# Kernel tuning notes

Measured on AMD Instinct MI355X. Metric: run time of the kernel, lower is better.

The kernel has to match this reference:

```python
import jax, jax.numpy as jnp
import numpy as np

N = 50000
E = 800000
IN = 256
H = 4
C = 64
HC = H * C
LAT = 64
EPS = 1e-5
NEG_SLOPE = 0.2


def setup_inputs() -> dict:
    key = jax.random.key(0)
    ks = jax.random.split(key, 20)
    g = lambda k, shape, fan: jax.random.normal(k, shape, jnp.float32) * (1.0 / np.sqrt(fan))
    return {
        "x": jax.random.normal(ks[0], (N, IN), jnp.float32),
        "edge_index": jax.random.randint(ks[1], (2, E), 0, N, jnp.int32),
        "Wl1": g(ks[2], (IN, HC), IN), "Wr1": g(ks[3], (IN, HC), IN),
        "att1": g(ks[4], (H, C), C), "b1": jnp.zeros((HC,), jnp.float32),
        "ln1_g": jnp.ones((HC,), jnp.float32), "ln1_b": jnp.zeros((HC,), jnp.float32),
        "Wl2": g(ks[5], (HC, HC), HC), "Wr2": g(ks[6], (HC, HC), HC),
        "att2": g(ks[7], (H, C), C), "b2": jnp.zeros((HC,), jnp.float32),
        "ln2_g": jnp.ones((HC,), jnp.float32), "ln2_b": jnp.zeros((HC,), jnp.float32),
        "Wmu": g(ks[8], (HC, LAT), HC), "bmu": jnp.zeros((LAT,), jnp.float32),
        "Wlv": g(ks[9], (HC, LAT), HC), "blv": jnp.zeros((LAT,), jnp.float32),
    }


def _gatv2_layer(x, src, dst, Wl, Wr, att, bias):
    # GATv2: e_ij = att . leaky_relu(Wl x_j + Wr x_i); segment softmax over dst; aggregate Wl x_j
    xl = (x @ Wl).reshape(-1, H, C)  # source transform [N,H,C]
    xr = (x @ Wr).reshape(-1, H, C)  # target transform [N,H,C]
    e = jax.nn.leaky_relu(xl[src] + xr[dst], NEG_SLOPE)   # [E',H,C]
    score = jnp.einsum('ehc,hc->eh', e, att)              # [E',H]
    m = jax.ops.segment_max(score, dst, num_segments=N)   # [N,H]
    ex = jnp.exp(score - m[dst])
    denom = jax.ops.segment_sum(ex, dst, num_segments=N)  # [N,H]
    alpha = ex / denom[dst]                               # self-loops guarantee denom > 0
    out = jax.ops.segment_sum(alpha[:, :, None] * xl[src], dst, num_segments=N)  # [N,H,C]
    return out.reshape(-1, HC) + bias


def _layernorm(x, g, b):
    mu = jnp.mean(x, axis=-1, keepdims=True)
    var = jnp.mean((x - mu) ** 2, axis=-1, keepdims=True)
    return (x - mu) * jax.lax.rsqrt(var + EPS) * g + b


def reference(x, edge_index, Wl1, Wr1, att1, b1, ln1_g, ln1_b,
              Wl2, Wr2, att2, b2, ln2_g, ln2_b, Wmu, bmu, Wlv, blv):
    loops = jnp.arange(N, dtype=edge_index.dtype)
    src = jnp.concatenate([edge_index[0], loops])  # add_self_loops=True
    dst = jnp.concatenate([edge_index[1], loops])
    h = _gatv2_layer(x, src, dst, Wl1, Wr1, att1, b1)
    h = jax.nn.elu(_layernorm(h, ln1_g, ln1_b))  # dropout is identity in eval mode
    h = _gatv2_layer(h, src, dst, Wl2, Wr2, att2, b2)
    h = jax.nn.elu(_layernorm(h, ln2_g, ln2_b))
    mu = h @ Wmu + bmu
    logvar = h @ Wlv + blv
    return mu, logvar
```

## Files before the change

kernel.cpp:

```cpp
#include <hip/hip_runtime.h>
#include <hip/hip_bf16.h>

#define NN 50000
#define NE 800000
#define HCn 256
#define LATn 64

typedef short bf16x4 __attribute__((ext_vector_type(4)));
typedef short bf16x8 __attribute__((ext_vector_type(8)));
typedef float f32x4 __attribute__((ext_vector_type(4)));

__device__ __forceinline__ short f2b(float f) {
    __hip_bfloat16 h = __float2bfloat16(f);
    return __builtin_bit_cast(short, h);
}
__device__ __forceinline__ float b2f(short s) {
    return __bfloat162float(__builtin_bit_cast(__hip_bfloat16, s));
}

#define SWZF(v, pat) __builtin_bit_cast(float, __builtin_amdgcn_ds_swizzle(__builtin_bit_cast(int, v), pat))

#define C04L2E 0.5770780163555854f
#define C06L2E 0.8656170245333781f
#define DEFER_THR 8.0f

__global__ void hist_kernel(const int* __restrict__ dst, int* __restrict__ counts) {
    int e = blockIdx.x * 256 + threadIdx.x;
    if (e < NE) atomicAdd(&counts[dst[e]], 1);
}

__global__ __launch_bounds__(1024) void scan1_kernel(int* __restrict__ counts,
                                                     int* __restrict__ blocksum) {
    const int g = blockIdx.x * 1024 + threadIdx.x;
    const int lane = threadIdx.x & 63;
    const int wv = threadIdx.x >> 6;
    int v = (g < NN) ? counts[g] : 0;
    int s = v;
#pragma unroll
    for (int d = 1; d < 64; d <<= 1) {
        int t = __shfl_up(s, d, 64);
        if (lane >= d) s += t;
    }
    __shared__ int wsum[16];
    if (lane == 63) wsum[wv] = s;
    __syncthreads();
    if (threadIdx.x == 0) {
        int run = 0;
#pragma unroll
        for (int q = 0; q < 16; ++q) { int t = wsum[q]; wsum[q] = run; run += t; }
        blocksum[blockIdx.x] = run;
    }
    __syncthreads();
    int excl = s - v + wsum[wv];
    if (g < NN) counts[g] = excl;
}

__global__ void scan2_kernel(int* __restrict__ blocksum, int* __restrict__ offsets, int nblk) {
    const int lane = threadIdx.x;
    int v = (lane < nblk) ? blocksum[lane] : 0;
    int s = v;
#pragma unroll
    for (int d = 1; d < 64; d <<= 1) {
        int t = __shfl_up(s, d, 64);
        if (lane >= d) s += t;
    }
    if (lane < nblk) blocksum[lane] = s - v;
    if (lane == 0) offsets[NN] = NE;
}

__global__ __launch_bounds__(1024) void scan3_kernel(const int* __restrict__ counts,
                                                     const int* __restrict__ blocksum,
                                                     int* __restrict__ offsets,
                                                     int* __restrict__ cursor) {
    const int g = blockIdx.x * 1024 + threadIdx.x;
    if (g < NN) {
        int v = counts[g] + blocksum[blockIdx.x];
        offsets[g] = v;
        cursor[g]  = v;
    }
}

__global__ void scatter_kernel(const int* __restrict__ src, const int* __restrict__ dst,
                               int* __restrict__ cursor, int* __restrict__ csr_src) {
    int e = blockIdx.x * 256 + threadIdx.x;
    if (e < NE) {
        int p = atomicAdd(&cursor[dst[e]], 1);
        csr_src[p] = src[e];
    }
}

__global__ void pack_w_kernel(const float* __restrict__ Wl1, const float* __restrict__ Wr1,
                              const float* __restrict__ Wl2, const float* __restrict__ Wr2,
                              const float* __restrict__ Wmu, const float* __restrict__ Wlv,
                              const float* __restrict__ bmu, const float* __restrict__ blv,
                              short* __restrict__ Wb1t, short* __restrict__ Wb2t,
                              short* __restrict__ Wb3t, float* __restrict__ bias3) {
    int i = blockIdx.x * 256 + threadIdx.x;
    const int S1 = 512 * 256, S2 = 2 * S1, S3 = S2 + 128 * 256;
    if (i < S1) {
        int c = i >> 8, k = i & 255;
        float v = (c < 256) ? Wl1[k * 256 + c] : Wr1[k * 256 + (c - 256)];
        Wb1t[i] = f2b(v);
    } else if (i < S2) {
        int j = i - S1; int c = j >> 8, k = j & 255;
        float v = (c < 256) ? Wl2[k * 256 + c] : Wr2[k * 256 + (c - 256)];
        Wb2t[j] = f2b(v);
    } else if (i < S3) {
        int j = i - S2; int c = j >> 8, k = j & 255;
        float v = (c < 64) ? Wmu[k * 64 + c] : Wlv[k * 64 + (c - 64)];
        Wb3t[j] = f2b(v);
    } else if (i < S3 + 128) {
        int c = i - S3;
        bias3[c] = (c < 64) ? bmu[c] : blv[c - 64];
    }
}

template<int A_F32, int OUT_MODE>
__global__ __launch_bounds__(256) void gemm_k(
    const void* __restrict__ Ap, const short* __restrict__ Wbt,
    void* __restrict__ outp, const float* __restrict__ bias, int Nc)
{
    __shared__ short Bs[128 * 256];
    const int t = threadIdx.x;
    const int w = t >> 6, lane = t & 63;
    const int row0 = blockIdx.x * 128, col0 = blockIdx.y * 128;

    {
        const int sn = t >> 1;
        const int half = t & 1;
        const short* wp = Wbt + (long)(col0 + sn) * 256 + half * 128;
        short* bp = &Bs[sn * 256];
        const int sx = sn & 7;
#pragma unroll
        for (int r = 0; r < 16; ++r) {
            bf16x8 v = *reinterpret_cast<const bf16x8*>(wp + r * 8);
            int c = half * 16 + r;
            *reinterpret_cast<bf16x8*>(bp + ((c ^ sx) * 8)) = v;
        }
    }
    __syncthreads();

    f32x4 acc[2][8];
#pragma unroll
    for (int a = 0; a < 2; ++a)
#pragma unroll
        for (int b = 0; b < 8; ++b) acc[a][b] = (f32x4){0.f, 0.f, 0.f, 0.f};

    const int arow = lane & 15, kq = lane >> 4;
    const int xorc = arow & 7;
    int r0 = row0 + w * 32 + arow;      if (r0 > NN - 1) r0 = NN - 1;
    int r1 = row0 + w * 32 + 16 + arow; if (r1 > NN - 1) r1 = NN - 1;

#pragma unroll
    for (int k0 = 0; k0 < 256; k0 += 32) {
        bf16x8 a0, a1;
        if (A_F32) {
            const float* A = (const float*)Ap;
            const f32x4* q0 = reinterpret_cast<const f32x4*>(A + (long)r0 * 256 + kq * 8 + k0);
            const f32x4* q1 = reinterpret_cast<const f32x4*>(A + (long)r1 * 256 + kq * 8 + k0);
            f32x4 u0 = q0[0], u1 = q0[1], v0 = q1[0], v1 = q1[1];
#pragma unroll
            for (int j = 0; j < 4; ++j) {
                a0[j] = f2b(u0[j]); a0[4 + j] = f2b(u1[j]);
                a1[j] = f2b(v0[j]); a1[4 + j] = f2b(v1[j]);
            }
        } else {
            const short* A = (const short*)Ap;
            a0 = *reinterpret_cast<const bf16x8*>(A + (long)r0 * 256 + kq * 8 + k0);
            a1 = *reinterpret_cast<const bf16x8*>(A + (long)r1 * 256 + kq * 8 + k0);
        }
        const int chunk = ((k0 >> 3) + kq) ^ xorc;
        const short* bsp = &Bs[arow * 256 + chunk * 8];
#pragma unroll
        for (int nt = 0; nt < 8; ++nt) {
            bf16x8 b = *reinterpret_cast<const bf16x8*>(bsp + nt * 4096);
            acc[0][nt] = __builtin_amdgcn_mfma_f32_16x16x32_bf16(a0, b, acc[0][nt], 0, 0, 0);
            acc[1][nt] = __builtin_amdgcn_mfma_f32_16x16x32_bf16(a1, b, acc[1][nt], 0, 0, 0);
        }
    }

#pragma unroll
    for (int rb = 0; rb < 2; ++rb)
#pragma unroll
        for (int nt = 0; nt < 8; ++nt) {
            int gcol = col0 + nt * 16 + arow;
#pragma unroll
            for (int r = 0; r < 4; ++r) {
                int grow = row0 + w * 32 + rb * 16 + kq * 4 + r;
                if (grow < NN) {
                    float v = acc[rb][nt][r];
                    if (OUT_MODE == 0) {
                        ((short*)outp)[(long)grow * Nc + gcol] = f2b(v);
                    } else {
                        v += bias[gcol];
                        float* o = (float*)outp;
                        if (gcol < 64) o[(long)grow * 64 + gcol] = v;
                        else           o[(long)NN * 64 + (long)grow * 64 + (gcol - 64)] = v;
                    }
                }
            }
        }
}

__global__ __launch_bounds__(256) void att_pre_kernel(
    const short* __restrict__ xlr, const float* __restrict__ att, float* __restrict__ a)
{
    const int i = blockIdx.x * 4 + (threadIdx.x >> 6);
    const int lane = threadIdx.x & 63;
    const int c4 = (lane >> 4) * 64 + (lane & 15) * 4;
    f32x4 attv = *reinterpret_cast<const f32x4*>(att + c4);
    bf16x4 v = *reinterpret_cast<const bf16x4*>(xlr + (long)i * 512 + c4);
    float s = 0.f;
#pragma unroll
    for (int k = 0; k < 4; ++k) s = fmaf(b2f(v[k]), attv[k], s);
    s += SWZF(s, 0x041F);
    s += SWZF(s, 0x081F);
    s += SWZF(s, 0x101F);
    s += SWZF(s, 0x201F);
    if ((lane & 15) == 0) a[i * 4 + (lane >> 4)] = s * C06L2E;
}

__device__ __forceinline__ void edge_abs_score(const short* __restrict__ xlr, int j, int c4,
                                               const float* xr, const f32x4& attv04,
                                               float* xf, float& s) {
    bf16x4 v = *reinterpret_cast<const bf16x4*>(xlr + (long)j * 512 + c4);
    s = 0.f;
#pragma unroll
    for (int k = 0; k < 4; ++k) {
        xf[k] = b2f(v[k]);
        float vv = xf[k] + xr[k];
        s = fmaf(attv04[k], fabsf(vv), s);
    }
    s += SWZF(s, 0x041F);
    s += SWZF(s, 0x081F);
    s += SWZF(s, 0x101F);
    s += SWZF(s, 0x201F);
}

__global__ __launch_bounds__(256) void gat_node_kernel(
    const short* __restrict__ xlr, const float* __restrict__ aarr,
    const int* __restrict__ offsets, const int* __restrict__ csr_src,
    const float* __restrict__ att, const float* __restrict__ bias,
    const float* __restrict__ ln_g, const float* __restrict__ ln_b,
    short* __restrict__ hout)
{
    const int i = blockIdx.x * 4 + (threadIdx.x >> 6);
    const int lane = threadIdx.x & 63;
    const int h  = lane >> 4;
    const int c4 = h * 64 + (lane & 15) * 4;

    f32x4 attv04 = *reinterpret_cast<const f32x4*>(att + c4);
#pragma unroll
    for (int k = 0; k < 4; ++k) attv04[k] *= C04L2E;

    float xr[4];
    {
        bf16x4 v = *reinterpret_cast<const bf16x4*>(xlr + (long)i * 512 + 256 + c4);
#pragma unroll
        for (int k = 0; k < 4; ++k) xr[k] = b2f(v[k]);
    }

    const int p0 = offsets[i], p1 = offsets[i + 1];

    int pp = p0 + (lane & 3);
    int jl = csr_src[pp < NE ? pp : NE - 1];

    float m, l;
    float acc[4];
    {
        float aj = aarr[i * 4 + h];
        float xf[4], s;
        edge_abs_score(xlr, i, c4, xr, attv04, xf, s);
        m = s + aj; l = 1.f;
#pragma unroll
        for (int k = 0; k < 4; ++k) acc[k] = xf[k];
    }

    int p = p0;
    for (; p + 4 <= p1; p += 4) {
        int j0 = __builtin_amdgcn_readlane(jl, 0);
        int j1 = __builtin_amdgcn_readlane(jl, 1);
        int j2 = __builtin_amdgcn_readlane(jl, 2);
        int j3 = __builtin_amdgcn_readlane(jl, 3);
        int pn = p + 4 + (lane & 3);
        jl = csr_src[pn < p1 ? pn : (p1 > 0 ? p1 - 1 : 0)];
        float a0 = aarr[j0 * 4 + h], a1 = aarr[j1 * 4 + h];
        float a2 = aarr[j2 * 4 + h], a3 = aarr[j3 * 4 + h];
        float x0[4], x1[4], x2[4], x3[4], s0, s1, s2, s3;
        edge_abs_score(xlr, j0, c4, xr, attv04, x0, s0);
        edge_abs_score(xlr, j1, c4, xr, attv04, x1, s1);
        edge_abs_score(xlr, j2, c4, xr, attv04, x2, s2);
        edge_abs_score(xlr, j3, c4, xr, attv04, x3, s3);
        s0 += a0; s1 += a1; s2 += a2; s3 += a3;
        float sm = fmaxf(fmaxf(s0, s1), fmaxf(s2, s3));
        if (__all(sm <= m + DEFER_THR)) {
            float e0 = __builtin_amdgcn_exp2f(s0 - m);
            float e1 = __builtin_amdgcn_exp2f(s1 - m);
            float e2 = __builtin_amdgcn_exp2f(s2 - m);
            float e3 = __builtin_amdgcn_exp2f(s3 - m);
            l += (e0 + e1) + (e2 + e3);
#pragma unroll
            for (int k = 0; k < 4; ++k)
                acc[k] = fmaf(e0, x0[k], fmaf(e1, x1[k], fmaf(e2, x2[k], fmaf(e3, x3[k], acc[k]))));
        } else {
            float mn = fmaxf(m, sm);
            float corr = __builtin_amdgcn_exp2f(m - mn);
            float e0 = __builtin_amdgcn_exp2f(s0 - mn);
            float e1 = __builtin_amdgcn_exp2f(s1 - mn);
            float e2 = __builtin_amdgcn_exp2f(s2 - mn);
            float e3 = __builtin_amdgcn_exp2f(s3 - mn);
            l = fmaf(l, corr, (e0 + e1) + (e2 + e3));
#pragma unroll
            for (int k = 0; k < 4; ++k)
                acc[k] = fmaf(acc[k], corr,
                         fmaf(e0, x0[k], fmaf(e1, x1[k], fmaf(e2, x2[k], e3 * x3[k]))));
            m = mn;
        }
    }
    int rem = p1 - p;
    for (int tq = 0; tq < rem; ++tq) {
        int j = __builtin_amdgcn_readlane(jl, tq);
        float aj = aarr[j * 4 + h];
        float xa[4], sa;
        edge_abs_score(xlr, j, c4, xr, attv04, xa, sa);
        sa += aj;
        if (__all(sa <= m + DEFER_THR)) {
            float ex = __builtin_amdgcn_exp2f(sa - m);
            l += ex;
#pragma unroll
            for (int k = 0; k < 4; ++k) acc[k] = fmaf(ex, xa[k], acc[k]);
        } else {
            float mn = fmaxf(m, sa);
            float corr = __builtin_amdgcn_exp2f(m - mn);
            float ex = __builtin_amdgcn_exp2f(sa - mn);
            l = fmaf(l, corr, ex);
#pragma unroll
            for (int k = 0; k < 4; ++k) acc[k] = fmaf(acc[k], corr, ex * xa[k]);
            m = mn;
        }
    }

    float inv = 1.f / l;
    f32x4 bv = *reinterpret_cast<const f32x4*>(bias + c4);
    float out[4], s1 = 0.f, s2 = 0.f;
#pragma unroll
    for (int k = 0; k < 4; ++k) {
        out[k] = acc[k] * inv + bv[k];
        s1 += out[k];
        s2 += out[k] * out[k];
    }
    s1 += SWZF(s1, 0x041F); s2 += SWZF(s2, 0x041F);
    s1 += SWZF(s1, 0x081F); s2 += SWZF(s2, 0x081F);
    s1 += SWZF(s1, 0x101F); s2 += SWZF(s2, 0x101F);
    s1 += SWZF(s1, 0x201F); s2 += SWZF(s2, 0x201F);
    s1 += SWZF(s1, 0x401F); s2 += SWZF(s2, 0x401F);
    s1 += __shfl_xor(s1, 32, 64);
    s2 += __shfl_xor(s2, 32, 64);
    float mu  = s1 * (1.f / 256.f);
    float var = s2 * (1.f / 256.f) - mu * mu;
    float rs  = rsqrtf(var + 1e-5f);
    f32x4 gv  = *reinterpret_cast<const f32x4*>(ln_g + c4);
    f32x4 bbv = *reinterpret_cast<const f32x4*>(ln_b + c4);
    bf16x4 o;
#pragma unroll
    for (int k = 0; k < 4; ++k) {
        float y = (out[k] - mu) * rs * gv[k] + bbv[k];
        y = y > 0.f ? y : expm1f(y);
        o[k] = f2b(y);
    }
    *reinterpret_cast<bf16x4*>(hout + (long)i * 256 + c4) = o;
}

extern "C" void kernel_launch(void* const* d_in, const int* in_sizes, int n_in,
                              void* d_out, int out_size, void* d_ws, size_t ws_size,
                              hipStream_t stream) {
    const float* x    = (const float*)d_in[0];
    const int*   ei   = (const int*)d_in[1];
    const float* Wl1  = (const float*)d_in[2];
    const float* Wr1  = (const float*)d_in[3];
    const float* att1 = (const float*)d_in[4];
    const float* b1   = (const float*)d_in[5];
    const float* ln1g = (const float*)d_in[6];
    const float* ln1b = (const float*)d_in[7];
    const float* Wl2  = (const float*)d_in[8];
    const float* Wr2  = (const float*)d_in[9];
    const float* att2 = (const float*)d_in[10];
    const float* b2   = (const float*)d_in[11];
    const float* ln2g = (const float*)d_in[12];
    const float* ln2b = (const float*)d_in[13];
    const float* Wmu  = (const float*)d_in[14];
    const float* bmu  = (const float*)d_in[15];
    const float* Wlv  = (const float*)d_in[16];
    const float* blv  = (const float*)d_in[17];

    short* bufXL = (short*)d_ws;
    short* bufH  = bufXL + (long)NN * 512;
    short* Wb1t  = bufH + (long)NN * 256;
    short* Wb2t  = Wb1t + 512 * 256;
    short* Wb3t  = Wb2t + 512 * 256;
    float* bias3 = (float*)(Wb3t + 128 * 256);
    int* counts  = (int*)(bias3 + 128);
    int* offsets = counts + NN;
    int* cursor  = offsets + NN + 1;
    int* csr_src = cursor + NN;
    int* blocksum = csr_src + NE;
    float* a_arr = (float*)(blocksum + 64);

    const int* src = ei;
    const int* dst = ei + NE;

    const int NBLK = (NN + 1023) / 1024;

    hipMemsetAsync(counts, 0, NN * sizeof(int), stream);
    hist_kernel<<<(NE + 255) / 256, 256, 0, stream>>>(dst, counts);
    scan1_kernel<<<NBLK, 1024, 0, stream>>>(counts, blocksum);
    scan2_kernel<<<1, 64, 0, stream>>>(blocksum, offsets, NBLK);
    scan3_kernel<<<NBLK, 1024, 0, stream>>>(counts, blocksum, offsets, cursor);
    scatter_kernel<<<(NE + 255) / 256, 256, 0, stream>>>(src, dst, cursor, csr_src);

    pack_w_kernel<<<1153, 256, 0, stream>>>(Wl1, Wr1, Wl2, Wr2, Wmu, Wlv, bmu, blv,
                                            Wb1t, Wb2t, Wb3t, bias3);

    const int GM = (NN + 127) / 128;
    dim3 g1(GM, 4);
    dim3 g3(GM, 1);

    gemm_k<1, 0><<<g1, 256, 0, stream>>>(x, Wb1t, bufXL, nullptr, 512);
    att_pre_kernel<<<NN / 4, 256, 0, stream>>>(bufXL, att1, a_arr);
    gat_node_kernel<<<NN / 4, 256, 0, stream>>>(bufXL, a_arr, offsets, csr_src,
                                                att1, b1, ln1g, ln1b, bufH);
    gemm_k<0, 0><<<g1, 256, 0, stream>>>(bufH, Wb2t, bufXL, nullptr, 512);
    att_pre_kernel<<<NN / 4, 256, 0, stream>>>(bufXL, att2, a_arr);
    gat_node_kernel<<<NN / 4, 256, 0, stream>>>(bufXL, a_arr, offsets, csr_src,
                                                att2, b2, ln2g, ln2b, bufH);
    gemm_k<0, 1><<<g3, 256, 0, stream>>>(bufH, Wb3t, d_out, bias3, 128);
}
```

Measured before the change: 374.0 us.

## Restructure GEMM to hold A rows in registers and fuse attention precompute

The GEMM now keeps each block's 64-row A tile in registers and loops over all output column tiles, staging a 64-column weight slice in shared memory per iteration. This replaces the earlier 2D grid that re-read A once per column tile. The separate att_pre kernel is removed: its per-node attention dot product is computed from the fp32 accumulators inside the GEMM epilogue, saving one launch and a re-read of the bf16 output per layer. In exchange, the column loop is serialised with a barrier per tile, there are fewer independent blocks, and the attention term now comes from unrounded fp32 values rather than the stored bf16 ones.

```diff
diff --git a/kernel.cpp b/kernel.cpp
--- a/kernel.cpp
+++ b/kernel.cpp
@@ -115,80 +115,98 @@
     }
 }
 
-template<int A_F32, int OUT_MODE>
+template<int A_F32, int OUT_MODE, int NCT, int ATT>
 __global__ __launch_bounds__(256) void gemm_k(
     const void* __restrict__ Ap, const short* __restrict__ Wbt,
-    void* __restrict__ outp, const float* __restrict__ bias, int Nc)
+    void* __restrict__ outp, const float* __restrict__ bias,
+    const float* __restrict__ att, float* __restrict__ a_arr, int Nc)
 {
-    __shared__ short Bs[128 * 256];
+    __shared__ short Bs[64 * 256];
     const int t = threadIdx.x;
     const int w = t >> 6, lane = t & 63;
-    const int row0 = blockIdx.x * 128, col0 = blockIdx.y * 128;
-
-    {
-        const int sn = t >> 1;
-        const int half = t & 1;
-        const short* wp = Wbt + (long)(col0 + sn) * 256 + half * 128;
-        short* bp = &Bs[sn * 256];
-        const int sx = sn & 7;
-#pragma unroll
-        for (int r = 0; r < 16; ++r) {
-            bf16x8 v = *reinterpret_cast<const bf16x8*>(wp + r * 8);
-            int c = half * 16 + r;
-            *reinterpret_cast<bf16x8*>(bp + ((c ^ sx) * 8)) = v;
-        }
-    }
-    __syncthreads();
-
-    f32x4 acc[2][8];
-#pragma unroll
-    for (int a = 0; a < 2; ++a)
-#pragma unroll
-        for (int b = 0; b < 8; ++b) acc[a][b] = (f32x4){0.f, 0.f, 0.f, 0.f};
-
+    const int row0 = blockIdx.x * 64;
     const int arow = lane & 15, kq = lane >> 4;
     const int xorc = arow & 7;
-    int r0 = row0 + w * 32 + arow;      if (r0 > NN - 1) r0 = NN - 1;
-    int r1 = row0 + w * 32 + 16 + arow; if (r1 > NN - 1) r1 = NN - 1;
-
-#pragma unroll
-    for (int k0 = 0; k0 < 256; k0 += 32) {
-        bf16x8 a0, a1;
+
+    bf16x8 af[8];
+    {
+        int r0 = row0 + w * 16 + arow; if (r0 > NN - 1) r0 = NN - 1;
         if (A_F32) {
             const float* A = (const float*)Ap;
-            const f32x4* q0 = reinterpret_cast<const f32x4*>(A + (long)r0 * 256 + kq * 8 + k0);
-            const f32x4* q1 = reinterpret_cast<const f32x4*>(A + (long)r1 * 256 + kq * 8 + k0);
-            f32x4 u0 = q0[0], u1 = q0[1], v0 = q1[0], v1 = q1[1];
-#pragma unroll
-            for (int j = 0; j < 4; ++j) {
-                a0[j] = f2b(u0[j]); a0[4 + j] = f2b(u1[j]);
-                a1[j] = f2b(v0[j]); a1[4 + j] = f2b(v1[j]);
+            const float* base = A + (long)r0 * 256 + kq * 8;
+#pragma unroll
+            for (int kc = 0; kc < 8; ++kc) {
+                const f32x4* q = reinterpret_cast<const f32x4*>(base + kc * 32);
+                f32x4 u0 = q[0], u1 = q[1];
+#pragma unroll
+                for (int j = 0; j < 4; ++j) { af[kc][j] = f2b(u0[j]); af[kc][4 + j] = f2b(u1[j]); }
             }
         } else {
             const short* A = (const short*)Ap;
-            a0 = *reinterpret_cast<const bf16x8*>(A + (long)r0 * 256 + kq * 8 + k0);
-            a1 = *reinterpret_cast<const bf16x8*>(A + (long)r1 * 256 + kq * 8 + k0);
-        }
-        const int chunk = ((k0 >> 3) + kq) ^ xorc;
-        const short* bsp = &Bs[arow * 256 + chunk * 8];
-#pragma unroll
-        for (int nt = 0; nt < 8; ++nt) {
-            bf16x8 b = *reinterpret_cast<const bf16x8*>(bsp + nt * 4096);
-            acc[0][nt] = __builtin_amdgcn_mfma_f32_16x16x32_bf16(a0, b, acc[0][nt], 0, 0, 0);
-            acc[1][nt] = __builtin_amdgcn_mfma_f32_16x16x32_bf16(a1, b, acc[1][nt], 0, 0, 0);
-        }
-    }
-
-#pragma unroll
-    for (int rb = 0; rb < 2; ++rb)
-#pragma unroll
-        for (int nt = 0; nt < 8; ++nt) {
-            int gcol = col0 + nt * 16 + arow;
+            const short* base = A + (long)r0 * 256 + kq * 8;
+#pragma unroll
+            for (int kc = 0; kc < 8; ++kc)
+                af[kc] = *reinterpret_cast<const bf16x8*>(base + kc * 32);
+        }
+    }
+
+    const int sn = t >> 2;
+    const int cq = t & 3;
+
+#pragma unroll 1
+    for (int ct = 0; ct < NCT; ++ct) {
+        {
+            const short* wp = Wbt + (long)(ct * 64 + sn) * 256;
+            short* bp = &Bs[sn * 256];
+            const int sx = sn & 7;
+#pragma unroll
+            for (int r = 0; r < 8; ++r) {
+                int c = cq + r * 4;
+                bf16x8 v = *reinterpret_cast<const bf16x8*>(wp + c * 8);
+                *reinterpret_cast<bf16x8*>(bp + ((c ^ sx) * 8)) = v;
+            }
+        }
+        __syncthreads();
+
+        f32x4 acc[4];
+#pragma unroll
+        for (int b = 0; b < 4; ++b) acc[b] = (f32x4){0.f, 0.f, 0.f, 0.f};
+
+#pragma unroll
+        for (int kc = 0; kc < 8; ++kc) {
+            const int chunk = (kc * 4 + kq) ^ xorc;
+#pragma unroll
+            for (int nt = 0; nt < 4; ++nt) {
+                bf16x8 b = *reinterpret_cast<const bf16x8*>(&Bs[(nt * 16 + arow) * 256 + chunk * 8]);
+                acc[nt] = __builtin_amdgcn_mfma_f32_16x16x32_bf16(af[kc], b, acc[nt], 0, 0, 0);
+            }
+        }
+
+        if (ATT && ct < 4) {
+            float av[4];
+#pragma unroll
+            for (int nt = 0; nt < 4; ++nt) av[nt] = att[ct * 64 + nt * 16 + arow];
 #pragma unroll
             for (int r = 0; r < 4; ++r) {
-                int grow = row0 + w * 32 + rb * 16 + kq * 4 + r;
+                float pd = av[0] * acc[0][r] + av[1] * acc[1][r]
+                         + av[2] * acc[2][r] + av[3] * acc[3][r];
+                pd += SWZF(pd, 0x041F);
+                pd += SWZF(pd, 0x081F);
+                pd += SWZF(pd, 0x101F);
+                pd += SWZF(pd, 0x201F);
+                int grow = row0 + w * 16 + kq * 4 + r;
+                if (arow == 0 && grow < NN) a_arr[grow * 4 + ct] = pd * C06L2E;
+            }
+        }
+
+#pragma unroll
+        for (int nt = 0; nt < 4; ++nt) {
+            int gcol = ct * 64 + nt * 16 + arow;
+#pragma unroll
+            for (int r = 0; r < 4; ++r) {
+                int grow = row0 + w * 16 + kq * 4 + r;
                 if (grow < NN) {
-                    float v = acc[rb][nt][r];
+                    float v = acc[nt][r];
                     if (OUT_MODE == 0) {
                         ((short*)outp)[(long)grow * Nc + gcol] = f2b(v);
                     } else {
@@ -200,24 +218,8 @@
                 }
             }
         }
-}
-
-__global__ __launch_bounds__(256) void att_pre_kernel(
-    const short* __restrict__ xlr, const float* __restrict__ att, float* __restrict__ a)
-{
-    const int i = blockIdx.x * 4 + (threadIdx.x >> 6);
-    const int lane = threadIdx.x & 63;
-    const int c4 = (lane >> 4) * 64 + (lane & 15) * 4;
-    f32x4 attv = *reinterpret_cast<const f32x4*>(att + c4);
-    bf16x4 v = *reinterpret_cast<const bf16x4*>(xlr + (long)i * 512 + c4);
-    float s = 0.f;
-#pragma unroll
-    for (int k = 0; k < 4; ++k) s = fmaf(b2f(v[k]), attv[k], s);
-    s += SWZF(s, 0x041F);
-    s += SWZF(s, 0x081F);
-    s += SWZF(s, 0x101F);
-    s += SWZF(s, 0x201F);
-    if ((lane & 15) == 0) a[i * 4 + (lane >> 4)] = s * C06L2E;
+        __syncthreads();
+    }
 }
 
 __device__ __forceinline__ void edge_abs_score(const short* __restrict__ xlr, int j, int c4,
@@ -421,17 +423,13 @@
     pack_w_kernel<<<1153, 256, 0, stream>>>(Wl1, Wr1, Wl2, Wr2, Wmu, Wlv, bmu, blv,
                                             Wb1t, Wb2t, Wb3t, bias3);
 
-    const int GM = (NN + 127) / 128;
-    dim3 g1(GM, 4);
-    dim3 g3(GM, 1);
-
-    gemm_k<1, 0><<<g1, 256, 0, stream>>>(x, Wb1t, bufXL, nullptr, 512);
-    att_pre_kernel<<<NN / 4, 256, 0, stream>>>(bufXL, att1, a_arr);
+    const int GM = (NN + 63) / 64;
+
+    gemm_k<1, 0, 8, 1><<<GM, 256, 0, stream>>>(x, Wb1t, bufXL, nullptr, att1, a_arr, 512);
     gat_node_kernel<<<NN / 4, 256, 0, stream>>>(bufXL, a_arr, offsets, csr_src,
                                                 att1, b1, ln1g, ln1b, bufH);
-    gemm_k<0, 0><<<g1, 256, 0, stream>>>(bufH, Wb2t, bufXL, nullptr, 512);
-    att_pre_kernel<<<NN / 4, 256, 0, stream>>>(bufXL, att2, a_arr);
+    gemm_k<0, 0, 8, 1><<<GM, 256, 0, stream>>>(bufH, Wb2t, bufXL, nullptr, att2, a_arr, 512);
     gat_node_kernel<<<NN / 4, 256, 0, stream>>>(bufXL, a_arr, offsets, csr_src,
                                                 att2, b2, ln2g, ln2b, bufH);
-    gemm_k<0, 1><<<g3, 256, 0, stream>>>(bufH, Wb3t, d_out, bias3, 128);
-}
+    gemm_k<0, 1, 2, 0><<<GM, 256, 0, stream>>>(bufH, Wb3t, d_out, bias3, nullptr, nullptr, 128);
+}
```

Result: faster. 333.6 us (-10.8%).
